# Kernel tuning notes

Hardware: AMD Instinct MI355X
Metric: run time of the kernel (lower is better)

The kernel has to match this reference:

```python
import jax, jax.numpy as jnp
import numpy as np

B, C, H, W = 8, 256, 48, 48
EPS = 1e-5


def _clinear(xr, xi, wr, wi, br, bi):
    # (Wr + iWi)(xr + ixi) + (br + ibi); torch Linear uses y = x @ W^T + b
    yr = jnp.einsum('bnc,dc->bnd', xr, wr) - jnp.einsum('bnc,dc->bnd', xi, wi) + br
    yi = jnp.einsum('bnc,dc->bnd', xr, wi) + jnp.einsum('bnc,dc->bnd', xi, wr) + bi
    return yr, yi


def _bn2d(x, w, b):
    # naive BatchNorm2d with batch statistics (biased var), per channel
    m = x.mean(axis=(0, 2, 3), keepdims=True)
    v = x.var(axis=(0, 2, 3), keepdims=True)
    return (x - m) * jax.lax.rsqrt(v + EPS) * w[None, :, None, None] + b[None, :, None, None]


def setup_inputs() -> dict:
    key = jax.random.key(0)
    ks = jax.random.split(key, 16)
    s = 1.0 / np.sqrt(C)
    inp = {
        'xr': jax.random.normal(ks[0], (B, C, H, W), jnp.float32),
        'xi': jax.random.normal(ks[1], (B, C, H, W), jnp.float32),
        'q_wr': jax.random.normal(ks[2], (C, C), jnp.float32) * s,
        'q_wi': jax.random.normal(ks[3], (C, C), jnp.float32) * s,
        'q_br': jax.random.normal(ks[4], (C,), jnp.float32) * s,
        'q_bi': jax.random.normal(ks[5], (C,), jnp.float32) * s,
        'k_wr': jax.random.normal(ks[6], (C, C), jnp.float32) * s,
        'k_wi': jax.random.normal(ks[7], (C, C), jnp.float32) * s,
        'k_br': jax.random.normal(ks[8], (C,), jnp.float32) * s,
        'k_bi': jax.random.normal(ks[9], (C,), jnp.float32) * s,
        'v_wr': jax.random.normal(ks[10], (C, C), jnp.float32) * s,
        'v_wi': jax.random.normal(ks[11], (C, C), jnp.float32) * s,
        'v_br': jax.random.normal(ks[12], (C,), jnp.float32) * s,
        'v_bi': jax.random.normal(ks[13], (C,), jnp.float32) * s,
        'gamma': jnp.float32(0.1),
        'bn_wr': jnp.ones((C,), jnp.float32),
        'bn_br': jnp.zeros((C,), jnp.float32),
        'bn_wi': jnp.ones((C,), jnp.float32),
        'bn_bi': jnp.zeros((C,), jnp.float32),
    }
    return inp


def reference(xr, xi, q_wr, q_wi, q_br, q_bi, k_wr, k_wi, k_br, k_bi,
              v_wr, v_wi, v_br, v_bi, gamma, bn_wr, bn_br, bn_wi, bn_bi):
    b, c, h, w = xr.shape
    n = h * w
    scale = jnp.float32(c) ** 0.5
    # [B,C,H,W] -> [B,N,C]
    xfr = xr.reshape(b, c, n).transpose(0, 2, 1)
    xfi = xi.reshape(b, c, n).transpose(0, 2, 1)
    qr, qi = _clinear(xfr, xfi, q_wr, q_wi, q_br, q_bi)
    kr, ki = _clinear(xfr, xfi, k_wr, k_wi, k_br, k_bi)
    vr, vi = _clinear(xfr, xfi, v_wr, v_wi, v_br, v_bi)
    # Re(Q @ conj(K)^T) = Qr Kr^T + Qi Ki^T  (imag part never used by module)
    attn_real = (jnp.einsum('bnc,bmc->bnm', qr, kr) +
                 jnp.einsum('bnc,bmc->bnm', qi, ki)) / scale
    a = jax.nn.softmax(attn_real, axis=-1)  # dropout: eval mode (identity)
    outr = jnp.einsum('bnm,bmc->bnc', a, vr)
    outi = jnp.einsum('bnm,bmc->bnc', a, vi)
    # [B,N,C] -> [B,C,H,W]
    outr = outr.transpose(0, 2, 1).reshape(b, c, h, w)
    outi = outi.transpose(0, 2, 1).reshape(b, c, h, w)
    yr = _bn2d(xr + gamma * outr, bn_wr, bn_br)
    yi = _bn2d(xi + gamma * outi, bn_wi, bn_bi)
    return jnp.stack([yr, yi], axis=0)  # [2,B,C,H,W] real/imag
```

## Files before the change

kernel.cpp:

```cpp
#include <hip/hip_runtime.h>
#include <cstdint>

#define NB 8
#define NC 256
#define NN 2304
#define NM (NB*NN)
#define EPS_ 1e-5f
#define LOG2E_ 1.44269504088896f

typedef __attribute__((ext_vector_type(8))) short bf16x8;
typedef __attribute__((ext_vector_type(8))) _Float16 f16x8;
typedef __attribute__((ext_vector_type(4))) _Float16 f16x4;
typedef __attribute__((ext_vector_type(4))) float f32x4;

__device__ __forceinline__ short f2bf(float x) {
    union { float f; uint32_t u; } v; v.f = x;
    uint32_t r = v.u + 0x7fffu + ((v.u >> 16) & 1u);
    return (short)(r >> 16);
}

#define MFMA_BF(a,b,c)  __builtin_amdgcn_mfma_f32_16x16x32_bf16(a,b,c,0,0,0)
#define MFMA_F16(a,b,c) __builtin_amdgcn_mfma_f32_16x16x32_f16(a,b,c,0,0,0)

#define GLOAD16(g,l) __builtin_amdgcn_global_load_lds( \
    (__attribute__((address_space(1))) void*)(g), \
    (__attribute__((address_space(3))) void*)(l), 16, 0, 0)

__global__ __launch_bounds__(256) void zero_accum(
    float* __restrict__ rowsum, float* __restrict__ csum, float* __restrict__ csum2)
{
    int i = blockIdx.x * 256 + threadIdx.x;
    if (i < NM) rowsum[i] = 0.f;
    if (i < 512) { csum[i] = 0.f; csum2[i] = 0.f; }
}

__global__ __launch_bounds__(256) void prepack_kernel(
    const float* __restrict__ q_wr, const float* __restrict__ q_wi,
    const float* __restrict__ q_br, const float* __restrict__ q_bi,
    const float* __restrict__ k_wr, const float* __restrict__ k_wi,
    const float* __restrict__ k_br, const float* __restrict__ k_bi,
    const float* __restrict__ v_wr, const float* __restrict__ v_wi,
    const float* __restrict__ v_br, const float* __restrict__ v_bi,
    short* __restrict__ Wcat, float* __restrict__ biasc)
{
    int idx = blockIdx.x * 256 + threadIdx.x;
    int g    = idx >> 17;
    int r    = idx & 131071;
    int d    = r >> 9;
    int k    = r & 511;
    int half = k >> 8;
    int kk   = k & 255;
    const float* wr_ = (g < 2) ? q_wr : (g < 4) ? k_wr : v_wr;
    const float* wi_ = (g < 2) ? q_wi : (g < 4) ? k_wi : v_wi;
    bool isR = (g & 1) == 0;
    const float* src = (half == 0) ? (isR ? wr_ : wi_) : (isR ? wi_ : wr_);
    float sign  = (half == 1 && isR) ? -1.f : 1.f;
    float scale = (g < 2) ? 0.0625f : 1.f;
    Wcat[idx] = f2bf(sign * scale * src[d * 256 + kk]);
    if (idx < 1536) {
        int gg = idx >> 8, dd = idx & 255;
        const float* bsrc = (gg==0)?q_br:(gg==1)?q_bi:(gg==2)?k_br:(gg==3)?k_bi:(gg==4)?v_br:v_bi;
        biasc[idx] = bsrc[dd] * ((gg < 2) ? 0.0625f : 1.f);
    }
}

__global__ __launch_bounds__(256) void xpose_cast(
    const float* __restrict__ xr, const float* __restrict__ xi,
    short* __restrict__ Xcat)
{
    __shared__ float t[32][33];
    int ri = blockIdx.z & 1, b = blockIdx.z >> 1;
    const float* src = (ri ? xi : xr) + (size_t)b * NC * NN;
    int n0 = blockIdx.x * 32, c0 = blockIdx.y * 32;
    int tx = threadIdx.x, ty = threadIdx.y;
    #pragma unroll
    for (int i = 0; i < 4; i++)
        t[ty + i*8][tx] = src[(size_t)(c0 + ty + i*8) * NN + n0 + tx];
    __syncthreads();
    #pragma unroll
    for (int i = 0; i < 4; i++) {
        int n = n0 + ty + i*8;
        Xcat[(size_t)(b * NN + n) * 512 + ri * 256 + c0 + tx] = f2bf(t[tx][ty + i*8]);
    }
}

__global__ __launch_bounds__(256, 3) void qkv_gemm(
    const short* __restrict__ Xcat, const short* __restrict__ Wcat,
    const float* __restrict__ biasc,
    short* __restrict__ QK, short* __restrict__ Vt)
{
    __shared__ short ldsA[128*64];
    __shared__ short ldsB[128*64];
    int tm = blockIdx.x;
    int tn = blockIdx.y;
    const short* Apanel = Xcat + (size_t)tm * 128 * 512;
    const short* Bpanel = Wcat + (size_t)tn * 128 * 512;
    int tid  = threadIdx.x;
    int lane = tid & 63, wid = tid >> 6;
    int li = lane & 15, lg = lane >> 4;
    int wr = wid >> 1, wc = wid & 1;
    int srow = tid >> 3, schk = tid & 7;

    f32x4 acc[4][4];
    #pragma unroll
    for (int i = 0; i < 4; i++)
        #pragma unroll
        for (int j = 0; j < 4; j++) acc[i][j] = (f32x4){0.f,0.f,0.f,0.f};

    for (int ks0 = 0; ks0 < 8; ks0++) {
        #pragma unroll
        for (int j = 0; j < 4; j++) {
            const short* ga = Apanel + (size_t)(j*32 + srow)*512 + ks0*64 + schk*8;
            const short* gb = Bpanel + (size_t)(j*32 + srow)*512 + ks0*64 + schk*8;
            GLOAD16(ga, ldsA + j*2048 + wid*512);
            GLOAD16(gb, ldsB + j*2048 + wid*512);
        }
        __syncthreads();
        #pragma unroll
        for (int ks = 0; ks < 2; ks++) {
            bf16x8 a[4], bv[4];
            #pragma unroll
            for (int i = 0; i < 4; i++) {
                a[i]  = *(const bf16x8*)&ldsA[(wr*64 + i*16 + li)*64 + ks*32 + lg*8];
                bv[i] = *(const bf16x8*)&ldsB[(wc*64 + i*16 + li)*64 + ks*32 + lg*8];
            }
            #pragma unroll
            for (int i = 0; i < 4; i++)
                #pragma unroll
                for (int j = 0; j < 4; j++)
                    acc[i][j] = MFMA_BF(a[i], bv[j], acc[i][j]);
        }
        __syncthreads();
    }

    if (tn < 8) {
        #pragma unroll
        for (int bj = 0; bj < 4; bj++) {
            int ncol = tn*128 + wc*64 + bj*16 + li;
            float bias = biasc[ncol];
            #pragma unroll
            for (int ai = 0; ai < 4; ai++)
                #pragma unroll
                for (int rr = 0; rr < 4; rr++) {
                    int m = tm*128 + wr*64 + ai*16 + lg*4 + rr;
                    QK[(size_t)m * 1024 + ncol] = f2bf(acc[ai][bj][rr] + bias);
                }
        }
    } else {
        int b  = tm / 18;
        int n0 = (tm - b*18) * 128 + wr*64;
        #pragma unroll
        for (int bj = 0; bj < 4; bj++) {
            int ncol = tn*128 + wc*64 + bj*16 + li;
            int cc = ncol - 1024;
            int ri2 = cc >> 8, c = cc & 255;
            float bias = biasc[ncol];
            short* vrow = Vt + ((size_t)((ri2*NB + b)*NC + c))*NN + n0;
            #pragma unroll
            for (int ai = 0; ai < 4; ai++) {
                f16x4 pk;
                #pragma unroll
                for (int rr = 0; rr < 4; rr++) pk[rr] = (_Float16)(acc[ai][bj][rr] + bias);
                *(f16x4*)(vrow + ai*16 + lg*4) = pk;
            }
        }
    }
}

__global__ __launch_bounds__(256, 3) void qk_gemm(
    const short* __restrict__ QK, _Float16* __restrict__ S,
    float* __restrict__ rowsum)
{
    __shared__ short ldsA[128*64];
    __shared__ short ldsB[128*64];
    int bi = blockIdx.x;
    int b  = bi & 7;
    int t  = bi >> 3;
    int tm = t % 18, tn = t / 18;
    const short* Abase = QK + ((size_t)b*NN + tm*128)*1024;
    const short* Bbase = QK + ((size_t)b*NN + tn*128)*1024 + 512;
    int tid  = threadIdx.x;
    int lane = tid & 63, wid = tid >> 6;
    int li = lane & 15, lg = lane >> 4;
    int wr = wid >> 1, wc = wid & 1;
    int srow = tid >> 3, schk = tid & 7;

    f32x4 acc[4][4];
    #pragma unroll
    for (int i = 0; i < 4; i++)
        #pragma unroll
        for (int j = 0; j < 4; j++) acc[i][j] = (f32x4){0.f,0.f,0.f,0.f};

    for (int ks0 = 0; ks0 < 8; ks0++) {
        #pragma unroll
        for (int j = 0; j < 4; j++) {
            const short* ga = Abase + (size_t)(j*32 + srow)*1024 + ks0*64 + schk*8;
            const short* gb = Bbase + (size_t)(j*32 + srow)*1024 + ks0*64 + schk*8;
            GLOAD16(ga, ldsA + j*2048 + wid*512);
            GLOAD16(gb, ldsB + j*2048 + wid*512);
        }
        __syncthreads();
        #pragma unroll
        for (int ks = 0; ks < 2; ks++) {
            bf16x8 a[4], bv[4];
            #pragma unroll
            for (int i = 0; i < 4; i++) {
                a[i]  = *(const bf16x8*)&ldsA[(wr*64 + i*16 + li)*64 + ks*32 + lg*8];
                bv[i] = *(const bf16x8*)&ldsB[(wc*64 + i*16 + li)*64 + ks*32 + lg*8];
            }
            #pragma unroll
            for (int i = 0; i < 4; i++)
                #pragma unroll
                for (int j = 0; j < 4; j++)
                    acc[i][j] = MFMA_BF(a[i], bv[j], acc[i][j]);
        }
        __syncthreads();
    }

    _Float16* Sb = S + ((size_t)b*NN + tm*128 + wr*64)*NN + tn*128 + wc*64;
    float psum[4][4];
    #pragma unroll
    for (int ai = 0; ai < 4; ai++)
        #pragma unroll
        for (int rr = 0; rr < 4; rr++) psum[ai][rr] = 0.f;
    #pragma unroll
    for (int ai = 0; ai < 4; ai++)
        #pragma unroll
        for (int bj = 0; bj < 4; bj++)
            #pragma unroll
            for (int rr = 0; rr < 4; rr++) {
                float p = exp2f((acc[ai][bj][rr] - 8.f) * LOG2E_);
                p = fminf(p, 60000.f);
                Sb[(size_t)(ai*16 + lg*4 + rr)*NN + bj*16 + li] = (_Float16)p;
                psum[ai][rr] += p;
            }
    #pragma unroll
    for (int ai = 0; ai < 4; ai++)
        #pragma unroll
        for (int rr = 0; rr < 4; rr++) {
            float s = psum[ai][rr];
            s += __shfl_xor(s, 1);
            s += __shfl_xor(s, 2);
            s += __shfl_xor(s, 4);
            s += __shfl_xor(s, 8);
            if (li == 0)
                atomicAdd(&rowsum[b*NN + tm*128 + wr*64 + ai*16 + lg*4 + rr], s);
        }
}

__global__ __launch_bounds__(256, 3) void pv_gemm(
    const short* __restrict__ Vt, const _Float16* __restrict__ P,
    const float* __restrict__ rowsum,
    const float* __restrict__ xr, const float* __restrict__ xi,
    const float* __restrict__ gamma_p,
    float* __restrict__ T, float* __restrict__ csum, float* __restrict__ csum2)
{
    __shared__ short ldsA[128*64];
    __shared__ short ldsB[128*64];
    int bi = blockIdx.x;
    int b  = bi & 7;
    int t  = bi >> 3;
    int tm = t & 3, tn = t >> 2;
    int ri = tm >> 1;
    int c0 = (tm & 1) * 128;
    const short*    Apanel = Vt + ((size_t)((ri*NB + b)*NC) + c0)*NN;
    const _Float16* Bpanel = P  + ((size_t)b*NN + tn*128)*NN;
    int tid  = threadIdx.x;
    int lane = tid & 63, wid = tid >> 6;
    int li = lane & 15, lg = lane >> 4;
    int wr = wid >> 1, wc = wid & 1;
    int srow = tid >> 3, schk = tid & 7;

    f32x4 acc[4][4];
    #pragma unroll
    for (int i = 0; i < 4; i++)
        #pragma unroll
        for (int j = 0; j < 4; j++) acc[i][j] = (f32x4){0.f,0.f,0.f,0.f};

    for (int ms = 0; ms < 36; ms++) {
        #pragma unroll
        for (int j = 0; j < 4; j++) {
            const short*    ga = Apanel + (size_t)(j*32 + srow)*NN + ms*64 + schk*8;
            const _Float16* gb = Bpanel + (size_t)(j*32 + srow)*NN + ms*64 + schk*8;
            GLOAD16(ga, ldsA + j*2048 + wid*512);
            GLOAD16(gb, ldsB + j*2048 + wid*512);
        }
        __syncthreads();
        #pragma unroll
        for (int ks = 0; ks < 2; ks++) {
            f16x8 a[4], bv[4];
            #pragma unroll
            for (int i = 0; i < 4; i++) {
                a[i]  = *(const f16x8*)&ldsA[(wr*64 + i*16 + li)*64 + ks*32 + lg*8];
                bv[i] = *(const f16x8*)&ldsB[(wc*64 + i*16 + li)*64 + ks*32 + lg*8];
            }
            #pragma unroll
            for (int i = 0; i < 4; i++)
                #pragma unroll
                for (int j = 0; j < 4; j++)
                    acc[i][j] = MFMA_F16(a[i], bv[j], acc[i][j]);
        }
        __syncthreads();
    }

    float gamma = gamma_p[0];
    const float* xsrc = (ri ? xi : xr) + (size_t)b * NC * NN;
    float* Tbase = T + (size_t)(ri*NB + b) * NC * NN;
    float linv[4];
    #pragma unroll
    for (int bj = 0; bj < 4; bj++)
        linv[bj] = 1.f / rowsum[b*NN + tn*128 + wc*64 + bj*16 + li];

    float s1[4][4], s2[4][4];
    #pragma unroll
    for (int ai = 0; ai < 4; ai++)
        #pragma unroll
        for (int rr = 0; rr < 4; rr++) { s1[ai][rr] = 0.f; s2[ai][rr] = 0.f; }

    #pragma unroll
    for (int ai = 0; ai < 4; ai++)
        #pragma unroll
        for (int rr = 0; rr < 4; rr++) {
            int c = c0 + wr*64 + ai*16 + lg*4 + rr;
            size_t roff = (size_t)c * NN + tn*128 + wc*64;
            #pragma unroll
            for (int bj = 0; bj < 4; bj++) {
                float tv = xsrc[roff + bj*16 + li] + gamma * (acc[ai][bj][rr] * linv[bj]);
                Tbase[roff + bj*16 + li] = tv;
                s1[ai][rr] += tv;
                s2[ai][rr] += tv * tv;
            }
        }
    #pragma unroll
    for (int ai = 0; ai < 4; ai++)
        #pragma unroll
        for (int rr = 0; rr < 4; rr++) {
            float a_ = s1[ai][rr], b_ = s2[ai][rr];
            a_ += __shfl_xor(a_, 1); b_ += __shfl_xor(b_, 1);
            a_ += __shfl_xor(a_, 2); b_ += __shfl_xor(b_, 2);
            a_ += __shfl_xor(a_, 4); b_ += __shfl_xor(b_, 4);
            a_ += __shfl_xor(a_, 8); b_ += __shfl_xor(b_, 8);
            if (li == 0) {
                int c = ri*NC + c0 + wr*64 + ai*16 + lg*4 + rr;
                atomicAdd(&csum[c], a_);
                atomicAdd(&csum2[c], b_);
            }
        }
}

__global__ __launch_bounds__(256) void finalize_stats(
    const float* __restrict__ csum, const float* __restrict__ csum2,
    float* __restrict__ mean_, float* __restrict__ rstd_)
{
    int i = blockIdx.x * 256 + threadIdx.x;
    if (i < 512) {
        float m = csum[i] * (1.f / 18432.f);
        float v = csum2[i] * (1.f / 18432.f) - m * m;
        mean_[i] = m;
        rstd_[i] = rsqrtf(v + EPS_);
    }
}

__global__ __launch_bounds__(256) void bn_apply(
    const float* __restrict__ T,
    const float* __restrict__ mean_, const float* __restrict__ rstd_,
    const float* __restrict__ bn_wr, const float* __restrict__ bn_br,
    const float* __restrict__ bn_wi, const float* __restrict__ bn_bi,
    float* __restrict__ out)
{
    size_t i4  = (size_t)blockIdx.x * 256 + threadIdx.x;
    size_t idx = i4 * 4;
    int g = (int)(idx / ((size_t)NB * NC * NN));
    size_t r1 = idx - (size_t)g * NB * NC * NN;
    int bc = (int)(r1 / NN);
    int c = bc & 255;
    float4 tv = *(const float4*)(T + idx);
    float m = mean_[g * NC + c], rs = rstd_[g * NC + c];
    float w = (g ? bn_wi : bn_wr)[c], bb = (g ? bn_bi : bn_br)[c];
    float a = rs * w;
    float4 y;
    y.x = (tv.x - m) * a + bb;
    y.y = (tv.y - m) * a + bb;
    y.z = (tv.z - m) * a + bb;
    y.w = (tv.w - m) * a + bb;
    *(float4*)(out + idx) = y;
}

extern "C" void kernel_launch(void* const* d_in, const int* in_sizes, int n_in,
                              void* d_out, int out_size, void* d_ws, size_t ws_size,
                              hipStream_t stream)
{
    const float* xr   = (const float*)d_in[0];
    const float* xi   = (const float*)d_in[1];
    const float* q_wr = (const float*)d_in[2];
    const float* q_wi = (const float*)d_in[3];
    const float* q_br = (const float*)d_in[4];
    const float* q_bi = (const float*)d_in[5];
    const float* k_wr = (const float*)d_in[6];
    const float* k_wi = (const float*)d_in[7];
    const float* k_br = (const float*)d_in[8];
    const float* k_bi = (const float*)d_in[9];
    const float* v_wr = (const float*)d_in[10];
    const float* v_wi = (const float*)d_in[11];
    const float* v_br = (const float*)d_in[12];
    const float* v_bi = (const float*)d_in[13];
    const float* gamma = (const float*)d_in[14];
    const float* bn_wr = (const float*)d_in[15];
    const float* bn_br = (const float*)d_in[16];
    const float* bn_wi = (const float*)d_in[17];
    const float* bn_bi = (const float*)d_in[18];
    float* out = (float*)d_out;

    char* p = (char*)d_ws;
    auto take = [&](size_t bytes) { char* q = p; p += (bytes + 255) & ~(size_t)255; return q; };
    short* Xcat  = (short*)take((size_t)NM * 512 * 2);
    short* Wcat  = (short*)take((size_t)1536 * 512 * 2);
    float* biasc = (float*)take(1536 * 4);
    short* QK    = (short*)take((size_t)NM * 1024 * 2);
    short* Vt    = (short*)take((size_t)2 * NB * NC * NN * 2);
    float* T     = (float*)take((size_t)2 * NB * NC * NN * 4);
    float* mean_ = (float*)take(512 * 4);
    float* rstd_ = (float*)take(512 * 4);
    _Float16* S  = (_Float16*)take((size_t)NB * NN * NN * 2);
    float* rowsum= (float*)take((size_t)NM * 4);
    float* csum  = (float*)take(512 * 4);
    float* csum2 = (float*)take(512 * 4);
    (void)ws_size; (void)in_sizes; (void)n_in; (void)out_size;

    zero_accum<<<72, 256, 0, stream>>>(rowsum, csum, csum2);
    prepack_kernel<<<3072, 256, 0, stream>>>(q_wr, q_wi, q_br, q_bi,
                                             k_wr, k_wi, k_br, k_bi,
                                             v_wr, v_wi, v_br, v_bi, Wcat, biasc);
    xpose_cast<<<dim3(72, 8, 16), dim3(32, 8), 0, stream>>>(xr, xi, Xcat);
    qkv_gemm<<<dim3(144, 12), 256, 0, stream>>>(Xcat, Wcat, biasc, QK, Vt);
    qk_gemm<<<18*18*8, 256, 0, stream>>>(QK, S, rowsum);
    pv_gemm<<<4*18*8, 256, 0, stream>>>(Vt, S, rowsum, xr, xi, gamma, T, csum, csum2);
    finalize_stats<<<2, 256, 0, stream>>>(csum, csum2, mean_, rstd_);
    bn_apply<<<9216, 256, 0, stream>>>(T, mean_, rstd_,
                                       bn_wr, bn_br, bn_wi, bn_bi, out);
}
```

Baseline: 253.9 us.

## Double-buffer LDS tiles and XOR-swizzle layout in QK and PV GEMMs

Both attention GEMMs now stage the next K/M slice into a second LDS buffer while the MFMAs run on the current one, so global-to-LDS loads overlap with compute. The global source column chunk is XOR-swizzled with the row index and the LDS reads apply the matching swizzle, which is meant to reduce bank conflicts on the 128-byte-stride row reads. LDS use doubles to 64 KB per block and launch bounds drop from 3 to 2 blocks per SM, which lowers occupancy.

```diff
diff --git a/kernel.cpp b/kernel.cpp
--- a/kernel.cpp
+++ b/kernel.cpp
@@ -167,12 +167,11 @@
     }
 }
 
-__global__ __launch_bounds__(256, 3) void qk_gemm(
+__global__ __launch_bounds__(256, 2) void qk_gemm(
     const short* __restrict__ QK, _Float16* __restrict__ S,
     float* __restrict__ rowsum)
 {
-    __shared__ short ldsA[128*64];
-    __shared__ short ldsB[128*64];
+    __shared__ short A0[128*64], B0[128*64], A1[128*64], B1[128*64];
     int bi = blockIdx.x;
     int b  = bi & 7;
     int t  = bi >> 3;
@@ -184,6 +183,7 @@
     int li = lane & 15, lg = lane >> 4;
     int wr = wid >> 1, wc = wid & 1;
     int srow = tid >> 3, schk = tid & 7;
+    int gsl = (schk ^ (srow & 7)) * 8;
 
     f32x4 acc[4][4];
     #pragma unroll
@@ -191,22 +191,24 @@
         #pragma unroll
         for (int j = 0; j < 4; j++) acc[i][j] = (f32x4){0.f,0.f,0.f,0.f};
 
-    for (int ks0 = 0; ks0 < 8; ks0++) {
+    auto stage = [&](short* sa, short* sb, int kk) {
         #pragma unroll
         for (int j = 0; j < 4; j++) {
-            const short* ga = Abase + (size_t)(j*32 + srow)*1024 + ks0*64 + schk*8;
-            const short* gb = Bbase + (size_t)(j*32 + srow)*1024 + ks0*64 + schk*8;
-            GLOAD16(ga, ldsA + j*2048 + wid*512);
-            GLOAD16(gb, ldsB + j*2048 + wid*512);
-        }
-        __syncthreads();
+            const short* ga = Abase + (size_t)(j*32 + srow)*1024 + kk*64 + gsl;
+            const short* gb = Bbase + (size_t)(j*32 + srow)*1024 + kk*64 + gsl;
+            GLOAD16(ga, sa + j*2048 + wid*512);
+            GLOAD16(gb, sb + j*2048 + wid*512);
+        }
+    };
+    auto compute = [&](const short* sa, const short* sb) {
         #pragma unroll
         for (int ks = 0; ks < 2; ks++) {
+            int so = ((ks*4 + lg) ^ (li & 7)) * 8;
             bf16x8 a[4], bv[4];
             #pragma unroll
             for (int i = 0; i < 4; i++) {
-                a[i]  = *(const bf16x8*)&ldsA[(wr*64 + i*16 + li)*64 + ks*32 + lg*8];
-                bv[i] = *(const bf16x8*)&ldsB[(wc*64 + i*16 + li)*64 + ks*32 + lg*8];
+                a[i]  = *(const bf16x8*)&sa[(wr*64 + i*16 + li)*64 + so];
+                bv[i] = *(const bf16x8*)&sb[(wc*64 + i*16 + li)*64 + so];
             }
             #pragma unroll
             for (int i = 0; i < 4; i++)
@@ -214,6 +216,16 @@
                 for (int j = 0; j < 4; j++)
                     acc[i][j] = MFMA_BF(a[i], bv[j], acc[i][j]);
         }
+    };
+
+    stage(A0, B0, 0);
+    __syncthreads();
+    for (int k0 = 0; k0 < 8; k0 += 2) {
+        stage(A1, B1, k0 + 1);
+        compute(A0, B0);
+        __syncthreads();
+        if (k0 + 2 < 8) stage(A0, B0, k0 + 2);
+        compute(A1, B1);
         __syncthreads();
     }
 
@@ -248,15 +260,14 @@
         }
 }
 
-__global__ __launch_bounds__(256, 3) void pv_gemm(
+__global__ __launch_bounds__(256, 2) void pv_gemm(
     const short* __restrict__ Vt, const _Float16* __restrict__ P,
     const float* __restrict__ rowsum,
     const float* __restrict__ xr, const float* __restrict__ xi,
     const float* __restrict__ gamma_p,
     float* __restrict__ T, float* __restrict__ csum, float* __restrict__ csum2)
 {
-    __shared__ short ldsA[128*64];
-    __shared__ short ldsB[128*64];
+    __shared__ short A0[128*64], B0[128*64], A1[128*64], B1[128*64];
     int bi = blockIdx.x;
     int b  = bi & 7;
     int t  = bi >> 3;
@@ -270,6 +281,7 @@
     int li = lane & 15, lg = lane >> 4;
     int wr = wid >> 1, wc = wid & 1;
     int srow = tid >> 3, schk = tid & 7;
+    int gsl = (schk ^ (srow & 7)) * 8;
 
     f32x4 acc[4][4];
     #pragma unroll
@@ -277,22 +289,24 @@
         #pragma unroll
         for (int j = 0; j < 4; j++) acc[i][j] = (f32x4){0.f,0.f,0.f,0.f};
 
-    for (int ms = 0; ms < 36; ms++) {
+    auto stage = [&](short* sa, short* sb, int mm) {
         #pragma unroll
         for (int j = 0; j < 4; j++) {
-            const short*    ga = Apanel + (size_t)(j*32 + srow)*NN + ms*64 + schk*8;
-            const _Float16* gb = Bpanel + (size_t)(j*32 + srow)*NN + ms*64 + schk*8;
-            GLOAD16(ga, ldsA + j*2048 + wid*512);
-            GLOAD16(gb, ldsB + j*2048 + wid*512);
-        }
-        __syncthreads();
+            const short*    ga = Apanel + (size_t)(j*32 + srow)*NN + mm*64 + gsl;
+            const _Float16* gb = Bpanel + (size_t)(j*32 + srow)*NN + mm*64 + gsl;
+            GLOAD16(ga, sa + j*2048 + wid*512);
+            GLOAD16(gb, sb + j*2048 + wid*512);
+        }
+    };
+    auto compute = [&](const short* sa, const short* sb) {
         #pragma unroll
         for (int ks = 0; ks < 2; ks++) {
+            int so = ((ks*4 + lg) ^ (li & 7)) * 8;
             f16x8 a[4], bv[4];
             #pragma unroll
             for (int i = 0; i < 4; i++) {
-                a[i]  = *(const f16x8*)&ldsA[(wr*64 + i*16 + li)*64 + ks*32 + lg*8];
-                bv[i] = *(const f16x8*)&ldsB[(wc*64 + i*16 + li)*64 + ks*32 + lg*8];
+                a[i]  = *(const f16x8*)&sa[(wr*64 + i*16 + li)*64 + so];
+                bv[i] = *(const f16x8*)&sb[(wc*64 + i*16 + li)*64 + so];
             }
             #pragma unroll
             for (int i = 0; i < 4; i++)
@@ -300,6 +314,16 @@
                 for (int j = 0; j < 4; j++)
                     acc[i][j] = MFMA_F16(a[i], bv[j], acc[i][j]);
         }
+    };
+
+    stage(A0, B0, 0);
+    __syncthreads();
+    for (int m0 = 0; m0 < 36; m0 += 2) {
+        stage(A1, B1, m0 + 1);
+        compute(A0, B0);
+        __syncthreads();
+        if (m0 + 2 < 36) stage(A0, B0, m0 + 2);
+        compute(A1, B1);
         __syncthreads();
     }
 
```

New measurement: 256.1 us. Within noise of the previous version (+0.8%).
